# Kernel optimization log

Hardware: AMD Instinct MI355X
Metric: run time of the kernel (lower is better)

The kernel has to match this reference:

```python
import jax, jax.numpy as jnp
import numpy as np

H_DIM = 2048
D_FF = 4 * H_DIM
NUM_EXPERTS = 8
NUM_SHARED = 2
BATCH, SEQ = 2, 2048


def setup_inputs() -> dict:
    key = jax.random.key(0)
    ks = jax.random.split(key, 10)
    s = 0.02
    return {
        "x": jax.random.normal(ks[0], (BATCH, SEQ, H_DIM), dtype=jnp.float32),
        "ws_w1": jax.random.normal(ks[1], (NUM_SHARED, H_DIM, D_FF), dtype=jnp.float32) * s,
        "ws_b1": jnp.zeros((NUM_SHARED, D_FF), dtype=jnp.float32),
        "ws_w2": jax.random.normal(ks[2], (NUM_SHARED, D_FF, H_DIM), dtype=jnp.float32) * s,
        "ws_b2": jnp.zeros((NUM_SHARED, H_DIM), dtype=jnp.float32),
        "we_w1": jax.random.normal(ks[3], (NUM_EXPERTS, H_DIM, D_FF), dtype=jnp.float32) * s,
        "we_b1": jnp.zeros((NUM_EXPERTS, D_FF), dtype=jnp.float32),
        "we_w2": jax.random.normal(ks[4], (NUM_EXPERTS, D_FF, H_DIM), dtype=jnp.float32) * s,
        "we_b2": jnp.zeros((NUM_EXPERTS, H_DIM), dtype=jnp.float32),
        "wg": jax.random.normal(ks[5], (H_DIM, NUM_EXPERTS), dtype=jnp.float32) * s,
        "top_k": 2,
    }


def reference(x, ws_w1, ws_b1, ws_w2, ws_b2, we_w1, we_b1, we_w2, we_b2, wg, top_k):
    B, S, D = x.shape
    xt = x.reshape(-1, D)  # [T, D], T = B*S
    T = xt.shape[0]

    # ---- shared experts: sum over NUM_SHARED dense MLPs ----
    hs = jax.nn.relu(jnp.einsum('td,ndf->ntf', xt, ws_w1) + ws_b1[:, None, :])
    shared = jnp.einsum('ntf,nfd->td', hs, ws_w2) + ws_b2.sum(axis=0)  # [T, D]

    # ---- sparse top-k routed MoE ----
    logits = xt @ wg                       # [T, E] router logits
    probs = jax.nn.softmax(logits, axis=-1)
    topv, topi = jax.lax.top_k(probs, top_k)
    gates = jnp.zeros_like(probs).at[jnp.arange(T)[:, None], topi].set(topv)  # [T, E]

    moe = jnp.zeros_like(xt)
    for e in range(we_w1.shape[0]):  # small fixed expert count
        he = jax.nn.relu(xt @ we_w1[e] + we_b1[e])
        ye = he @ we_w2[e] + we_b2[e]
        moe = moe + gates[:, e:e + 1] * ye

    out = (shared + moe).reshape(B, S, D)
    return out, logits
```

## Files before the change

### kernel.cpp

```cpp
#include <hip/hip_runtime.h>

#define TOKENS 4096
#define HD 2048
#define FF 8192
#define NE 8
#define NS 2

typedef __attribute__((ext_vector_type(8))) short bf16x8;
typedef __attribute__((ext_vector_type(4))) float f32x4;

__device__ __forceinline__ unsigned rnd_bf(unsigned u) {
  return u + 0x7fffu + ((u >> 16) & 1u);
}
__device__ __forceinline__ unsigned short f2bf(float f) {
  unsigned u = __builtin_bit_cast(unsigned, f);
  return (unsigned short)(rnd_bf(u) >> 16);
}

#define GLDS16(gp, lp)                                                         \
  __builtin_amdgcn_global_load_lds(                                            \
      (const __attribute__((address_space(1))) unsigned*)(const void*)(gp),    \
      (__attribute__((address_space(3))) unsigned*)(lp), 16, 0, 0)

__global__ void cast_x_kernel(const float* __restrict__ x, unsigned short* __restrict__ xb) {
  const size_t i = ((size_t)blockIdx.x * 256 + threadIdx.x) * 4;
  float4 v = *(const float4*)(x + i);
  ushort4 o;
  o.x = f2bf(v.x); o.y = f2bf(v.y); o.z = f2bf(v.z); o.w = f2bf(v.w);
  *(ushort4*)(xb + i) = o;
}

__global__ void router_kernel(const float* __restrict__ x, const float* __restrict__ wg,
                              float* __restrict__ logits_out, int* __restrict__ topi,
                              float* __restrict__ topv, int* __restrict__ counts) {
  const int wave = threadIdx.x >> 6, lane = threadIdx.x & 63;
  const int t = blockIdx.x * 4 + wave;
  const float* xr = x + (size_t)t * HD;
  float acc[8];
#pragma unroll
  for (int e = 0; e < 8; ++e) acc[e] = 0.f;
  for (int d = lane; d < HD; d += 64) {
    const float xv = xr[d];
    const float4 w0 = *(const float4*)(wg + (size_t)d * 8);
    const float4 w1 = *(const float4*)(wg + (size_t)d * 8 + 4);
    acc[0] += xv * w0.x; acc[1] += xv * w0.y; acc[2] += xv * w0.z; acc[3] += xv * w0.w;
    acc[4] += xv * w1.x; acc[5] += xv * w1.y; acc[6] += xv * w1.z; acc[7] += xv * w1.w;
  }
#pragma unroll
  for (int e = 0; e < 8; ++e) {
#pragma unroll
    for (int off = 32; off > 0; off >>= 1) acc[e] += __shfl_xor(acc[e], off);
  }
  if (lane == 0) {
    *(float4*)(logits_out + (size_t)t * 8)     = make_float4(acc[0], acc[1], acc[2], acc[3]);
    *(float4*)(logits_out + (size_t)t * 8 + 4) = make_float4(acc[4], acc[5], acc[6], acc[7]);
    float mx = acc[0];
#pragma unroll
    for (int e = 1; e < 8; ++e) mx = fmaxf(mx, acc[e]);
    float p[8], s = 0.f;
#pragma unroll
    for (int e = 0; e < 8; ++e) { p[e] = expf(acc[e] - mx); s += p[e]; }
    const float inv = 1.f / s;
    int i1 = 0;
#pragma unroll
    for (int e = 1; e < 8; ++e) if (acc[e] > acc[i1]) i1 = e;
    int i2 = (i1 == 0) ? 1 : 0;
#pragma unroll
    for (int e = 0; e < 8; ++e) if (e != i1 && acc[e] > acc[i2]) i2 = e;
    topi[2 * t]     = i1; topv[2 * t]     = p[i1] * inv;
    topi[2 * t + 1] = i2; topv[2 * t + 1] = p[i2] * inv;
    atomicAdd(&counts[i1], 1);
    atomicAdd(&counts[i2], 1);
  }
}

__global__ void offs_kernel(const int* __restrict__ counts, int* __restrict__ offs,
                            int* __restrict__ cursors) {
  if (threadIdx.x == 0) {
    int r = 0;
    for (int e = 0; e < NE; ++e) { offs[e] = r; cursors[e] = r; r += counts[e]; }
  }
}

__global__ void gather_kernel(const unsigned short* __restrict__ xb,
                              const int* __restrict__ topi, const float* __restrict__ topv,
                              int* __restrict__ cursors, unsigned short* __restrict__ xg,
                              int* __restrict__ row_token, float* __restrict__ row_gate,
                              int* __restrict__ row_of) {
  const int wave = threadIdx.x >> 6, lane = threadIdx.x & 63;
  const int t = blockIdx.x * 4 + wave;
  const uint4* src = (const uint4*)(xb + (size_t)t * HD);
#pragma unroll
  for (int j = 0; j < 2; ++j) {
    const int e = topi[2 * t + j];
    int pos = 0;
    if (lane == 0) {
      pos = atomicAdd(&cursors[e], 1);
      row_token[pos] = t;
      row_gate[pos] = topv[2 * t + j];
      row_of[2 * t + j] = pos;
    }
    pos = __shfl(pos, 0);
    uint4* dst = (uint4*)(xg + (size_t)pos * HD);
#pragma unroll
    for (int c = lane; c < 256; c += 64) dst[c] = src[c];
  }
}

template <int K, int N>
__global__ __launch_bounds__(256) void pack_wt(const float* __restrict__ we,
                                               const float* __restrict__ ws,
                                               unsigned short* __restrict__ dstw) {
  const int e = blockIdx.z;
  const float* src = (e < NE) ? (we + (size_t)e * K * N) : (ws + (size_t)(e - NE) * K * N);
  unsigned short* dst = dstw + (size_t)e * K * N;
  const int nt = blockIdx.x * 64;
  const int kt = blockIdx.y * 64;
  __shared__ unsigned short t[64][73];
  const int tid = threadIdx.x;
  const int rr = tid >> 4, cc = (tid & 15) * 4;
#pragma unroll
  for (int i = 0; i < 4; ++i) {
    const int k = rr + i * 16;
    float4 v = *(const float4*)(src + (size_t)(kt + k) * N + nt + cc);
    t[k][cc + 0] = f2bf(v.x);
    t[k][cc + 1] = f2bf(v.y);
    t[k][cc + 2] = f2bf(v.z);
    t[k][cc + 3] = f2bf(v.w);
  }
  __syncthreads();
  const int nr = tid >> 2, kc = (tid & 3) * 16;
  unsigned u[8];
#pragma unroll
  for (int j = 0; j < 8; ++j)
    u[j] = (unsigned)t[kc + 2 * j][nr] | ((unsigned)t[kc + 2 * j + 1][nr] << 16);
  unsigned short* dp = dst + (size_t)(nt + nr) * K + kt + kc;
  uint4 v0; v0.x = u[0]; v0.y = u[1]; v0.z = u[2]; v0.w = u[3];
  uint4 v1; v1.x = u[4]; v1.y = u[5]; v1.z = u[6]; v1.w = u[7];
  *(uint4*)dp = v0;
  *(uint4*)(dp + 8) = v1;
}

template <int MS>
__device__ __forceinline__ void rd_a(bf16x8 (&d)[8], const unsigned short* base,
                                     int wr, int fr, int fq, int swz) {
#pragma unroll
  for (int mi = 0; mi < 4; ++mi)
#pragma unroll
    for (int ks = 0; ks < 2; ++ks)
      d[mi * 2 + ks] = *(const bf16x8*)(base + (wr * 128 + MS * 64 + mi * 16 + fr) * 64 +
                                        (((ks * 4 + fq) ^ swz) << 3));
}
template <int NSUB>
__device__ __forceinline__ void rd_b(bf16x8 (&d)[4], const unsigned short* base,
                                     int wc, int fr, int fq, int swz) {
#pragma unroll
  for (int ni = 0; ni < 2; ++ni)
#pragma unroll
    for (int ks = 0; ks < 2; ++ks)
      d[ni * 2 + ks] = *(const bf16x8*)(base + (wc * 64 + NSUB * 32 + ni * 16 + fr) * 64 +
                                        (((ks * 4 + fq) ^ swz) << 3));
}
template <int MS, int NSUB>
__device__ __forceinline__ void mm16(f32x4 (&acc)[8][4], const bf16x8 (&a)[8],
                                     const bf16x8 (&b)[4]) {
  __builtin_amdgcn_s_setprio(1);
#pragma unroll
  for (int mi = 0; mi < 4; ++mi)
#pragma unroll
    for (int ni = 0; ni < 2; ++ni)
#pragma unroll
      for (int ks = 0; ks < 2; ++ks)
        acc[MS * 4 + mi][NSUB * 2 + ni] = __builtin_amdgcn_mfma_f32_16x16x32_bf16(
            a[mi * 2 + ks], b[ni * 2 + ks], acc[MS * 4 + mi][NSUB * 2 + ni], 0, 0, 0);
  __builtin_amdgcn_s_setprio(0);
}

#define PH_BAR_PRE()                                                           \
  __builtin_amdgcn_sched_barrier(0);                                           \
  __builtin_amdgcn_s_barrier();                                                \
  asm volatile("s_waitcnt lgkmcnt(0)" ::: "memory");                           \
  __builtin_amdgcn_sched_barrier(0)
#define PH_BAR_POST()                                                          \
  __builtin_amdgcn_sched_barrier(0);                                           \
  __builtin_amdgcn_s_barrier()

template <int K>
__device__ __forceinline__ void kloop(
    const unsigned short* __restrict__ A, const unsigned short* __restrict__ Bt,
    unsigned short* smem, int m0, int n0, f32x4 (&acc)[8][4],
    int wr, int wc, int fr, int fq, int swz,
    int wrA, int wcB, int lr8, int lc8, int scol) {
#define SAK(s, kt, b)                                                          \
  { const int r0_ = wrA + (s) * 64 + lr8;                                      \
    const unsigned short* s_ = A + (size_t)(m0 + r0_) * K + (kt) * 64 + scol;  \
    unsigned short* d_ = smem + (b) * 32768 + r0_ * 64 + lc8 * 8;              \
    GLDS16(s_, d_); GLDS16(s_ + (size_t)8 * K, d_ + 8 * 64); }
#define SBK(s, kt, b)                                                          \
  { const int r0_ = wcB + (s) * 32 + lr8;                                      \
    const unsigned short* s_ = Bt + (size_t)(n0 + r0_) * K + (kt) * 64 + scol; \
    unsigned short* d_ = smem + (b) * 32768 + 16384 + r0_ * 64 + lc8 * 8;      \
    GLDS16(s_, d_); GLDS16(s_ + (size_t)8 * K, d_ + 8 * 64); }

  SAK(0, 0, 0); SAK(1, 0, 0); SBK(0, 0, 0); SBK(1, 0, 0);
  SAK(0, 1, 1); SAK(1, 1, 1); SBK(0, 1, 1); SBK(1, 1, 1);
  asm volatile("s_waitcnt vmcnt(8)" ::: "memory");
  __builtin_amdgcn_s_barrier();

  bf16x8 a0[8], a1[8], b0[4], b1[4];
  rd_a<0>(a0, smem, wr, fr, fq, swz);
  rd_b<0>(b0, smem + 16384, wc, fr, fq, swz);

  const int nkt = K / 64;
  for (int t = 0; t < nkt; ++t) {
    const int cur = t & 1;
    const int tp2 = (t + 2 < nkt) ? t + 2 : t;
    const unsigned short* As_c = smem + cur * 32768;
    const unsigned short* Bs_c = As_c + 16384;
    const unsigned short* As_n = smem + (cur ^ 1) * 32768;
    const unsigned short* Bs_n = As_n + 16384;
    rd_b<1>(b1, Bs_c, wc, fr, fq, swz);
    mm16<0, 0>(acc, a0, b0);
    rd_a<1>(a1, As_c, wr, fr, fq, swz);
    mm16<0, 1>(acc, a0, b1);
    asm volatile("s_waitcnt lgkmcnt(0)" ::: "memory");
    __builtin_amdgcn_s_barrier();
    __builtin_amdgcn_sched_barrier(0);
    SAK(0, tp2, cur); SBK(0, tp2, cur);
    mm16<1, 0>(acc, a1, b0);
    asm volatile("s_waitcnt vmcnt(4)" ::: "memory");
    __builtin_amdgcn_s_barrier();
    __builtin_amdgcn_sched_barrier(0);
    rd_a<0>(a0, As_n, wr, fr, fq, swz);
    rd_b<0>(b0, Bs_n, wc, fr, fq, swz);
    SAK(1, tp2, cur); SBK(1, tp2, cur);
    mm16<1, 1>(acc, a1, b1);
  }
#undef SAK
#undef SBK
}

__global__ __launch_bounds__(512, 2) void g1k(
    const unsigned short* __restrict__ Ash, const unsigned short* __restrict__ Art,
    const unsigned short* __restrict__ wt1,
    const float* __restrict__ bE, const float* __restrict__ bS,
    unsigned short* __restrict__ hout,
    const int* __restrict__ counts, const int* __restrict__ offs,
    int do_pack, const float* __restrict__ we_w2, const float* __restrict__ ws_w2,
    unsigned short* __restrict__ wt2) {
  constexpr int K = HD;
  constexpr int NBX = FF / 256;
  constexpr int NWG = NBX * 16;
  extern __shared__ unsigned short smem[];

  const int e = blockIdx.z;
  int M;
  const unsigned short* A;
  const float* bias;
  int hbase;
  if (e < NE) {
    M = counts[e];
    A = Art + (size_t)offs[e] * K;
    bias = bE + (size_t)e * FF;
    hbase = offs[e];
  } else {
    M = TOKENS;
    A = Ash;
    bias = bS + (size_t)(e - NE) * FF;
    hbase = 2 * TOKENS + (e - NE) * TOKENS;
  }
  const unsigned short* Bt = wt1 + (size_t)e * HD * FF;

  int flat = blockIdx.x + NBX * blockIdx.y;
  flat = (flat & 7) * (NWG >> 3) + (flat >> 3);
  const int m0 = (flat & 15) * 256;
  const int n0 = (flat >> 4) * 256;
  const int tid = threadIdx.x;

  if (m0 >= M) {
    if (!do_pack) return;
    int total = 0, prefix = 0;
    for (int e2 = 0; e2 < NE; ++e2) {
      int mb = (counts[e2] + 255) >> 8; if (mb > 16) mb = 16;
      const int inv = 32 * (16 - mb);
      if (e2 < e) prefix += inv;
      total += inv;
    }
    int mb_e = (counts[e] + 255) >> 8; if (mb_e > 16) mb_e = 16;
    const int m_idx = flat & 15, n_idx = flat >> 4;
    const int rank = prefix + n_idx * (16 - mb_e) + (m_idx - mb_e);
    unsigned short* ps = smem;
    const int NT = 10 * 128 * 32;
    int it = 0;
    for (int i = rank; i < NT; i += total, ++it) {
      const int e2 = i >> 12;
      const int rem = i & 4095;
      const int ktt = rem >> 5;
      const int ntt = rem & 31;
      const float* src = (e2 < NE) ? (we_w2 + (size_t)e2 * FF * HD)
                                   : (ws_w2 + (size_t)(e2 - NE) * FF * HD);
      unsigned short* dst = wt2 + (size_t)e2 * HD * FF;
      unsigned short* pb = ps + (it & 1) * (64 * 73);
      {
        const int kk = tid >> 3, cc = (tid & 7) * 8;
        const float* sp = src + (size_t)(ktt * 64 + kk) * HD + ntt * 64 + cc;
        const float4 v0 = *(const float4*)sp;
        const float4 v1 = *(const float4*)(sp + 4);
        unsigned short* tp = pb + kk * 73 + cc;
        tp[0] = f2bf(v0.x); tp[1] = f2bf(v0.y); tp[2] = f2bf(v0.z); tp[3] = f2bf(v0.w);
        tp[4] = f2bf(v1.x); tp[5] = f2bf(v1.y); tp[6] = f2bf(v1.z); tp[7] = f2bf(v1.w);
      }
      __syncthreads();
      {
        const int nn = tid >> 3, kc = (tid & 7) * 8;
        unsigned u[4];
#pragma unroll
        for (int j = 0; j < 4; ++j)
          u[j] = (unsigned)pb[(kc + 2 * j) * 73 + nn] |
                 ((unsigned)pb[(kc + 2 * j + 1) * 73 + nn] << 16);
        uint4 v; v.x = u[0]; v.y = u[1]; v.z = u[2]; v.w = u[3];
        *(uint4*)(dst + (size_t)(ntt * 64 + nn) * FF + ktt * 64 + kc) = v;
      }
    }
    return;
  }

  const int wid = tid >> 6, ln = tid & 63;
  const int wr = wid >> 2, wc = wid & 3;
  const int fr = ln & 15, fq = ln >> 4;
  const int swz = fr & 7;
  const int lr8 = ln >> 3;
  const int lc8 = ln & 7;
  const int scol = (lc8 ^ lr8) << 3;
  const int wrA = wr * 128 + wc * 16;
  const int wcB = wc * 64 + wr * 16;

  f32x4 acc[8][4];
#pragma unroll
  for (int i = 0; i < 8; ++i)
#pragma unroll
    for (int j = 0; j < 4; ++j) acc[i][j] = (f32x4){0.f, 0.f, 0.f, 0.f};

  kloop<K>(A, Bt, smem, m0, n0, acc, wr, wc, fr, fq, swz, wrA, wcB, lr8, lc8, scol);

#pragma unroll
  for (int nn = 0; nn < 4; ++nn) {
#pragma unroll
    for (int mm = 0; mm < 8; ++mm) {
      const int col = n0 + wc * 64 + (nn >> 1) * 32 + (nn & 1) * 16 + fr;
      const float bb = bias[col];
#pragma unroll
      for (int j = 0; j < 4; ++j) {
        const int r = m0 + wr * 128 + (mm >> 2) * 64 + (mm & 3) * 16 + fq * 4 + j;
        if (r < M) {
          float v = acc[mm][nn][j] + bb;
          v = v > 0.f ? v : 0.f;
          hout[(size_t)(hbase + r) * FF + col] = f2bf(v);
        }
      }
    }
  }
}

__global__ __launch_bounds__(512, 2) void g2k(
    const unsigned short* __restrict__ hbuf, const unsigned short* __restrict__ wt2,
    const float* __restrict__ bE, const float* __restrict__ bS,
    float* __restrict__ ybuf,
    const int* __restrict__ counts, const int* __restrict__ offs) {
  constexpr int K = FF;
  constexpr int NBX = HD / 256;
  constexpr int NWG = NBX * 16;
  extern __shared__ unsigned short smem[];

  const int e = blockIdx.z;
  int M;
  const unsigned short* A;
  const float* bias;
  int hbase;
  if (e < NE) {
    M = counts[e];
    A = hbuf + (size_t)offs[e] * K;
    bias = bE + (size_t)e * HD;
    hbase = offs[e];
  } else {
    M = TOKENS;
    hbase = 2 * TOKENS + (e - NE) * TOKENS;
    A = hbuf + (size_t)hbase * K;
    bias = bS + (size_t)(e - NE) * HD;
  }
  const unsigned short* Bt = wt2 + (size_t)e * HD * FF;

  int flat = blockIdx.x + NBX * blockIdx.y;
  flat = (flat & 7) * (NWG >> 3) + (flat >> 3);
  const int m0 = (flat & 15) * 256;
  const int n0 = (flat >> 4) * 256;
  if (m0 >= M) return;

  const int tid = threadIdx.x;
  const int wid = tid >> 6, ln = tid & 63;
  const int wr = wid >> 2, wc = wid & 3;
  const int fr = ln & 15, fq = ln >> 4;
  const int swz = fr & 7;
  const int lr8 = ln >> 3;
  const int lc8 = ln & 7;
  const int scol = (lc8 ^ lr8) << 3;
  const int wrA = wr * 128 + wc * 16;
  const int wcB = wc * 64 + wr * 16;

  f32x4 acc[8][4];
#pragma unroll
  for (int i = 0; i < 8; ++i)
#pragma unroll
    for (int j = 0; j < 4; ++j) acc[i][j] = (f32x4){0.f, 0.f, 0.f, 0.f};

  kloop<K>(A, Bt, smem, m0, n0, acc, wr, wc, fr, fq, swz, wrA, wcB, lr8, lc8, scol);

#pragma unroll
  for (int nn = 0; nn < 4; ++nn) {
#pragma unroll
    for (int mm = 0; mm < 8; ++mm) {
      const int colw = wc * 64 + (nn >> 1) * 32 + (nn & 1) * 16 + fr;
      const float bb = bias[n0 + colw];
#pragma unroll
      for (int j = 0; j < 4; ++j) {
        const int r = m0 + wr * 128 + (mm >> 2) * 64 + (mm & 3) * 16 + fq * 4 + j;
        if (r < M)
          ybuf[(size_t)(hbase + r) * HD + n0 + colw] = acc[mm][nn][j] + bb;
      }
    }
  }
}

__global__ __launch_bounds__(256) void reduce_kernel(
    const float* __restrict__ ybuf, const int* __restrict__ row_of,
    const float* __restrict__ topv, float* __restrict__ out) {
  const int t = blockIdx.x;
  const int d = threadIdx.x * 8;
  const float g0 = topv[2 * t], g1 = topv[2 * t + 1];
  const float* y0 = ybuf + (size_t)row_of[2 * t] * HD + d;
  const float* y1 = ybuf + (size_t)row_of[2 * t + 1] * HD + d;
  const float* s0 = ybuf + (size_t)(2 * TOKENS + t) * HD + d;
  const float* s1 = ybuf + (size_t)(3 * TOKENS + t) * HD + d;
  float* o = out + (size_t)t * HD + d;
#pragma unroll
  for (int q = 0; q < 2; ++q) {
    const float4 a = *(const float4*)(s0 + q * 4);
    const float4 b = *(const float4*)(s1 + q * 4);
    const float4 c = *(const float4*)(y0 + q * 4);
    const float4 e = *(const float4*)(y1 + q * 4);
    float4 r;
    r.x = a.x + b.x + g0 * c.x + g1 * e.x;
    r.y = a.y + b.y + g0 * c.y + g1 * e.y;
    r.z = a.z + b.z + g0 * c.z + g1 * e.z;
    r.w = a.w + b.w + g0 * c.w + g1 * e.w;
    *(float4*)(o + q * 4) = r;
  }
}

extern "C" void kernel_launch(void* const* d_in, const int* in_sizes, int n_in,
                              void* d_out, int out_size, void* d_ws, size_t ws_size,
                              hipStream_t stream) {
  const float* x     = (const float*)d_in[0];
  const float* ws_w1 = (const float*)d_in[1];
  const float* ws_b1 = (const float*)d_in[2];
  const float* ws_w2 = (const float*)d_in[3];
  const float* ws_b2 = (const float*)d_in[4];
  const float* we_w1 = (const float*)d_in[5];
  const float* we_b1 = (const float*)d_in[6];
  const float* we_w2 = (const float*)d_in[7];
  const float* we_b2 = (const float*)d_in[8];
  const float* wg    = (const float*)d_in[9];

  float* out = (float*)d_out;
  float* logits = out + (size_t)TOKENS * HD;

  hipFuncSetAttribute(reinterpret_cast<const void*>(g1k),
                      hipFuncAttributeMaxDynamicSharedMemorySize, 131072);
  hipFuncSetAttribute(reinterpret_cast<const void*>(g2k),
                      hipFuncAttributeMaxDynamicSharedMemorySize, 131072);

  char* ws = (char*)d_ws;
  unsigned short* wt1  = (unsigned short*)ws;
  unsigned short* wt2  = (unsigned short*)(ws + 335544320);
  unsigned short* xb   = (unsigned short*)(ws + 671088640);
  unsigned short* xg   = (unsigned short*)(ws + 687865856);
  unsigned short* hbuf = (unsigned short*)(ws + 721944576);
  char* ctrl = ws + 990380032;
  float* ybuf = (float*)ws;
  int*   row_token = (int*)(ctrl);
  float* row_gate  = (float*)(ctrl + 32768);
  int*   topi      = (int*)(ctrl + 65536);
  float* topv      = (float*)(ctrl + 98304);
  int*   counts    = (int*)(ctrl + 131072);
  int*   offs      = (int*)(ctrl + 131104);
  int*   cursors   = (int*)(ctrl + 131136);
  int*   row_of    = (int*)(ctrl + 131168);

  hipMemsetAsync(counts, 0, NE * sizeof(int), stream);
  cast_x_kernel<<<8192, 256, 0, stream>>>(x, xb);
  router_kernel<<<1024, 256, 0, stream>>>(x, wg, logits, topi, topv, counts);
  offs_kernel<<<1, 64, 0, stream>>>(counts, offs, cursors);
  gather_kernel<<<1024, 256, 0, stream>>>(xb, topi, topv, cursors, xg,
                                          row_token, row_gate, row_of);
  pack_wt<HD, FF><<<dim3(FF / 64, HD / 64, 10), 256, 0, stream>>>(we_w1, ws_w1, wt1);
  g1k<<<dim3(32, 16, 10), 512, 131072, stream>>>(
      xb, xg, wt1, we_b1, ws_b1, hbuf, counts, offs, 1, we_w2, ws_w2, wt2);
  g2k<<<dim3(8, 16, 10), 512, 131072, stream>>>(
      hbuf, wt2, we_b2, ws_b2, ybuf, counts, offs);
  reduce_kernel<<<TOKENS, 256, 0, stream>>>(ybuf, row_of, topv, out);

  (void)in_sizes; (void)n_in; (void)out_size; (void)ws_size;
}
```

Baseline: 1.875 ms.

## Split-K the second GEMM into two halves and prefetch weight-pack loads

The second expert GEMM (K=8192) is split into two K halves launched as extra grid z-slices. Each half writes its own partial output buffer, with the bias added only in the first half, and the reduce kernel sums both halves. This doubles the number of workgroups, so the GPU is better filled when few expert tiles are active, at the cost of extra partial-result writes and reads. The w2 pack/transposing path in g1k's idle blocks is also software-pipelined so the next tile's global loads are issued before the current tile is converted.

```diff
diff --git a/kernel.cpp b/kernel.cpp
--- a/kernel.cpp
+++ b/kernel.cpp
@@ -5,6 +5,7 @@
 #define FF 8192
 #define NE 8
 #define NS 2
+#define YHALF 33554432
 
 typedef __attribute__((ext_vector_type(8))) short bf16x8;
 typedef __attribute__((ext_vector_type(4))) float f32x4;
@@ -176,21 +177,12 @@
   __builtin_amdgcn_s_setprio(0);
 }
 
-#define PH_BAR_PRE()                                                           \
-  __builtin_amdgcn_sched_barrier(0);                                           \
-  __builtin_amdgcn_s_barrier();                                                \
-  asm volatile("s_waitcnt lgkmcnt(0)" ::: "memory");                           \
-  __builtin_amdgcn_sched_barrier(0)
-#define PH_BAR_POST()                                                          \
-  __builtin_amdgcn_sched_barrier(0);                                           \
-  __builtin_amdgcn_s_barrier()
-
 template <int K>
 __device__ __forceinline__ void kloop(
     const unsigned short* __restrict__ A, const unsigned short* __restrict__ Bt,
     unsigned short* smem, int m0, int n0, f32x4 (&acc)[8][4],
     int wr, int wc, int fr, int fq, int swz,
-    int wrA, int wcB, int lr8, int lc8, int scol) {
+    int wrA, int wcB, int lr8, int lc8, int scol, int kt0, int nkt) {
 #define SAK(s, kt, b)                                                          \
   { const int r0_ = wrA + (s) * 64 + lr8;                                      \
     const unsigned short* s_ = A + (size_t)(m0 + r0_) * K + (kt) * 64 + scol;  \
@@ -202,8 +194,8 @@
     unsigned short* d_ = smem + (b) * 32768 + 16384 + r0_ * 64 + lc8 * 8;      \
     GLDS16(s_, d_); GLDS16(s_ + (size_t)8 * K, d_ + 8 * 64); }
 
-  SAK(0, 0, 0); SAK(1, 0, 0); SBK(0, 0, 0); SBK(1, 0, 0);
-  SAK(0, 1, 1); SAK(1, 1, 1); SBK(0, 1, 1); SBK(1, 1, 1);
+  SAK(0, kt0, 0); SAK(1, kt0, 0); SBK(0, kt0, 0); SBK(1, kt0, 0);
+  SAK(0, kt0 + 1, 1); SAK(1, kt0 + 1, 1); SBK(0, kt0 + 1, 1); SBK(1, kt0 + 1, 1);
   asm volatile("s_waitcnt vmcnt(8)" ::: "memory");
   __builtin_amdgcn_s_barrier();
 
@@ -211,10 +203,9 @@
   rd_a<0>(a0, smem, wr, fr, fq, swz);
   rd_b<0>(b0, smem + 16384, wc, fr, fq, swz);
 
-  const int nkt = K / 64;
   for (int t = 0; t < nkt; ++t) {
     const int cur = t & 1;
-    const int tp2 = (t + 2 < nkt) ? t + 2 : t;
+    const int tp2 = kt0 + ((t + 2 < nkt) ? t + 2 : t);
     const unsigned short* As_c = smem + cur * 32768;
     const unsigned short* Bs_c = As_c + 16384;
     const unsigned short* As_n = smem + (cur ^ 1) * 32768;
@@ -291,27 +282,37 @@
     const int rank = prefix + n_idx * (16 - mb_e) + (m_idx - mb_e);
     unsigned short* ps = smem;
     const int NT = 10 * 128 * 32;
-    int it = 0;
-    for (int i = rank; i < NT; i += total, ++it) {
-      const int e2 = i >> 12;
-      const int rem = i & 4095;
-      const int ktt = rem >> 5;
-      const int ntt = rem & 31;
+    const int kk = tid >> 3, cc = (tid & 7) * 8;
+    float4 r0a, r0b;
+    int i = rank;
+    if (i < NT) {
+      const int e2 = i >> 12, rem = i & 4095, ktt = rem >> 5, ntt = rem & 31;
       const float* src = (e2 < NE) ? (we_w2 + (size_t)e2 * FF * HD)
                                    : (ws_w2 + (size_t)(e2 - NE) * FF * HD);
-      unsigned short* dst = wt2 + (size_t)e2 * HD * FF;
+      const float* sp = src + (size_t)(ktt * 64 + kk) * HD + ntt * 64 + cc;
+      r0a = *(const float4*)sp; r0b = *(const float4*)(sp + 4);
+    }
+    int it = 0;
+    while (i < NT) {
+      const int inext = i + total;
+      float4 r1a, r1b;
+      if (inext < NT) {
+        const int e2 = inext >> 12, rem = inext & 4095, ktt = rem >> 5, ntt = rem & 31;
+        const float* src = (e2 < NE) ? (we_w2 + (size_t)e2 * FF * HD)
+                                     : (ws_w2 + (size_t)(e2 - NE) * FF * HD);
+        const float* sp = src + (size_t)(ktt * 64 + kk) * HD + ntt * 64 + cc;
+        r1a = *(const float4*)sp; r1b = *(const float4*)(sp + 4);
+      }
       unsigned short* pb = ps + (it & 1) * (64 * 73);
       {
-        const int kk = tid >> 3, cc = (tid & 7) * 8;
-        const float* sp = src + (size_t)(ktt * 64 + kk) * HD + ntt * 64 + cc;
-        const float4 v0 = *(const float4*)sp;
-        const float4 v1 = *(const float4*)(sp + 4);
         unsigned short* tp = pb + kk * 73 + cc;
-        tp[0] = f2bf(v0.x); tp[1] = f2bf(v0.y); tp[2] = f2bf(v0.z); tp[3] = f2bf(v0.w);
-        tp[4] = f2bf(v1.x); tp[5] = f2bf(v1.y); tp[6] = f2bf(v1.z); tp[7] = f2bf(v1.w);
+        tp[0] = f2bf(r0a.x); tp[1] = f2bf(r0a.y); tp[2] = f2bf(r0a.z); tp[3] = f2bf(r0a.w);
+        tp[4] = f2bf(r0b.x); tp[5] = f2bf(r0b.y); tp[6] = f2bf(r0b.z); tp[7] = f2bf(r0b.w);
       }
       __syncthreads();
       {
+        const int e2 = i >> 12, rem = i & 4095, ktt = rem >> 5, ntt = rem & 31;
+        unsigned short* dst = wt2 + (size_t)e2 * HD * FF;
         const int nn = tid >> 3, kc = (tid & 7) * 8;
         unsigned u[4];
 #pragma unroll
@@ -321,6 +322,8 @@
         uint4 v; v.x = u[0]; v.y = u[1]; v.z = u[2]; v.w = u[3];
         *(uint4*)(dst + (size_t)(ntt * 64 + nn) * FF + ktt * 64 + kc) = v;
       }
+      r0a = r1a; r0b = r1b;
+      i = inext; ++it;
     }
     return;
   }
@@ -341,7 +344,8 @@
 #pragma unroll
     for (int j = 0; j < 4; ++j) acc[i][j] = (f32x4){0.f, 0.f, 0.f, 0.f};
 
-  kloop<K>(A, Bt, smem, m0, n0, acc, wr, wc, fr, fq, swz, wrA, wcB, lr8, lc8, scol);
+  kloop<K>(A, Bt, smem, m0, n0, acc, wr, wc, fr, fq, swz, wrA, wcB, lr8, lc8, scol,
+           0, K / 64);
 
 #pragma unroll
   for (int nn = 0; nn < 4; ++nn) {
@@ -372,7 +376,9 @@
   constexpr int NWG = NBX * 16;
   extern __shared__ unsigned short smem[];
 
-  const int e = blockIdx.z;
+  const int z = blockIdx.z;
+  const int e = (z < 10) ? z : z - 10;
+  const int half = (z < 10) ? 0 : 1;
   int M;
   const unsigned short* A;
   const float* bias;
@@ -389,6 +395,7 @@
     bias = bS + (size_t)(e - NE) * HD;
   }
   const unsigned short* Bt = wt2 + (size_t)e * HD * FF;
+  float* yout = ybuf + (size_t)half * YHALF;
 
   int flat = blockIdx.x + NBX * blockIdx.y;
   flat = (flat & 7) * (NWG >> 3) + (flat >> 3);
@@ -413,19 +420,20 @@
 #pragma unroll
     for (int j = 0; j < 4; ++j) acc[i][j] = (f32x4){0.f, 0.f, 0.f, 0.f};
 
-  kloop<K>(A, Bt, smem, m0, n0, acc, wr, wc, fr, fq, swz, wrA, wcB, lr8, lc8, scol);
+  kloop<K>(A, Bt, smem, m0, n0, acc, wr, wc, fr, fq, swz, wrA, wcB, lr8, lc8, scol,
+           half * 64, 64);
 
 #pragma unroll
   for (int nn = 0; nn < 4; ++nn) {
 #pragma unroll
     for (int mm = 0; mm < 8; ++mm) {
       const int colw = wc * 64 + (nn >> 1) * 32 + (nn & 1) * 16 + fr;
-      const float bb = bias[n0 + colw];
+      const float bb = (half == 0) ? bias[n0 + colw] : 0.f;
 #pragma unroll
       for (int j = 0; j < 4; ++j) {
         const int r = m0 + wr * 128 + (mm >> 2) * 64 + (mm & 3) * 16 + fq * 4 + j;
         if (r < M)
-          ybuf[(size_t)(hbase + r) * HD + n0 + colw] = acc[mm][nn][j] + bb;
+          yout[(size_t)(hbase + r) * HD + n0 + colw] = acc[mm][nn][j] + bb;
       }
     }
   }
@@ -437,22 +445,26 @@
   const int t = blockIdx.x;
   const int d = threadIdx.x * 8;
   const float g0 = topv[2 * t], g1 = topv[2 * t + 1];
-  const float* y0 = ybuf + (size_t)row_of[2 * t] * HD + d;
-  const float* y1 = ybuf + (size_t)row_of[2 * t + 1] * HD + d;
-  const float* s0 = ybuf + (size_t)(2 * TOKENS + t) * HD + d;
-  const float* s1 = ybuf + (size_t)(3 * TOKENS + t) * HD + d;
+  const size_t r0 = (size_t)row_of[2 * t] * HD + d;
+  const size_t r1 = (size_t)row_of[2 * t + 1] * HD + d;
+  const size_t rs0 = (size_t)(2 * TOKENS + t) * HD + d;
+  const size_t rs1 = (size_t)(3 * TOKENS + t) * HD + d;
   float* o = out + (size_t)t * HD + d;
 #pragma unroll
   for (int q = 0; q < 2; ++q) {
-    const float4 a = *(const float4*)(s0 + q * 4);
-    const float4 b = *(const float4*)(s1 + q * 4);
-    const float4 c = *(const float4*)(y0 + q * 4);
-    const float4 e = *(const float4*)(y1 + q * 4);
-    float4 r;
-    r.x = a.x + b.x + g0 * c.x + g1 * e.x;
-    r.y = a.y + b.y + g0 * c.y + g1 * e.y;
-    r.z = a.z + b.z + g0 * c.z + g1 * e.z;
-    r.w = a.w + b.w + g0 * c.w + g1 * e.w;
+    float4 r = {0.f, 0.f, 0.f, 0.f};
+#pragma unroll
+    for (int h = 0; h < 2; ++h) {
+      const float* yb = ybuf + (size_t)h * YHALF;
+      const float4 a = *(const float4*)(yb + rs0 + q * 4);
+      const float4 b = *(const float4*)(yb + rs1 + q * 4);
+      const float4 c = *(const float4*)(yb + r0 + q * 4);
+      const float4 ee = *(const float4*)(yb + r1 + q * 4);
+      r.x += a.x + b.x + g0 * c.x + g1 * ee.x;
+      r.y += a.y + b.y + g0 * c.y + g1 * ee.y;
+      r.z += a.z + b.z + g0 * c.z + g1 * ee.z;
+      r.w += a.w + b.w + g0 * c.w + g1 * ee.w;
+    }
     *(float4*)(o + q * 4) = r;
   }
 }
@@ -505,7 +517,7 @@
   pack_wt<HD, FF><<<dim3(FF / 64, HD / 64, 10), 256, 0, stream>>>(we_w1, ws_w1, wt1);
   g1k<<<dim3(32, 16, 10), 512, 131072, stream>>>(
       xb, xg, wt1, we_b1, ws_b1, hbuf, counts, offs, 1, we_w2, ws_w2, wt2);
-  g2k<<<dim3(8, 16, 10), 512, 131072, stream>>>(
+  g2k<<<dim3(8, 16, 20), 512, 131072, stream>>>(
       hbuf, wt2, we_b2, ws_b2, ybuf, counts, offs);
   reduce_kernel<<<TOKENS, 256, 0, stream>>>(ybuf, row_of, topv, out);
 
```

After: 1.867 ms. No clear change (-0.4%).
